# Kernel tuning notes

Measured on AMD Instinct MI355X. Metric: run time of the kernel, lower is better.

Reference implementation:

```python
import jax, jax.numpy as jnp
import numpy as np

B, S, I, H, C, V = 512, 64, 300, 1024, 2, 50000


def setup_inputs() -> dict:
    key = jax.random.key(0)
    ks = jax.random.split(key, 10)
    s = 0.05
    return {
        "x": jax.random.randint(ks[0], (B, S), 0, V),
        "lengths": jax.random.randint(ks[1], (B,), 1, S + 1),
        "embed": jax.random.normal(ks[2], (V, I), jnp.float32) * s,
        "Wih_e": jax.random.normal(ks[3], (4 * H, I), jnp.float32) * s,
        "Whh_e": jax.random.normal(ks[4], (4 * H, H), jnp.float32) * s,
        "bih_e": jnp.zeros((4 * H,), jnp.float32),
        "bhh_e": jnp.zeros((4 * H,), jnp.float32),
        "Wih_d": jax.random.normal(ks[5], (4 * H, I), jnp.float32) * s,
        "Whh_d": jax.random.normal(ks[6], (4 * H, H), jnp.float32) * s,
        "bih_d": jnp.zeros((4 * H,), jnp.float32),
        "bhh_d": jnp.zeros((4 * H,), jnp.float32),
        "W_lin": jax.random.normal(ks[7], (C, H), jnp.float32) * s,
        "b_lin": jnp.zeros((C,), jnp.float32),
    }


def lstm_cell(xi, h, c, Wih, Whh, bih, bhh):
    # PyTorch LSTMCell gate order: i, f, g, o
    g = xi @ Wih.T + bih + h @ Whh.T + bhh
    i, f, gg, o = jnp.split(g, 4, axis=-1)
    c = jax.nn.sigmoid(f) * c + jax.nn.sigmoid(i) * jnp.tanh(gg)
    return jax.nn.sigmoid(o) * jnp.tanh(c), c


def reference(x, lengths, embed, Wih_e, Whh_e, bih_e, bhh_e,
              Wih_d, Whh_d, bih_d, bhh_d, W_lin, b_lin):
    bsz, slen = x.shape
    hdim = Whh_e.shape[1]
    ncls = W_lin.shape[0]
    xs = embed[x.T]                      # [S, B, I] (seq-major, like x.transpose(0,1))

    h0 = jnp.zeros((bsz, hdim), xs.dtype)
    c0 = jnp.zeros((bsz, hdim), xs.dtype)

    def enc_step(carry, xi):
        h, c = carry
        h, c = lstm_cell(xi, h, c, Wih_e, Whh_e, bih_e, bhh_e)
        return (h, c), h

    # forward pass over sequence
    (h, c), enc_fwd = jax.lax.scan(enc_step, (h0, c0), xs)          # enc_fwd: [S,B,H]
    # backward pass with the SAME encoder cell, continuing from (h, c)
    (h, c), h_bwd = jax.lax.scan(enc_step, (h, c), xs[::-1])        # h_bwd:  [S,B,H]
    # k-th backward step pairs with encoder_forward[k] in the original code
    enc_out = (enc_fwd + h_bwd) * 0.5                               # [S,B,H]

    def dec_step(carry, xi):
        h, c = carry
        # original attention sums over batch AND hidden -> one scalar per timestep,
        # and rebuilds w as a fresh Variable (no gradient through the weights).
        w = jax.nn.softmax(jnp.sum(h[None, :, :] * enc_out, axis=(1, 2)))  # [S]
        w = jax.lax.stop_gradient(w)
        h = h + jnp.einsum('t,tbh->bh', w, enc_out)
        h, c = lstm_cell(xi, h, c, Wih_d, Whh_d, bih_d, bhh_d)
        return (h, c), h

    _, dec = jax.lax.scan(dec_step, (h, c), xs)                     # [S,B,H]

    out = dec @ W_lin.T + b_lin                                     # [S,B,C]
    out = out.transpose(1, 0, 2)                                    # [B,S,C]
    pad = jnp.array([1.0, 0.0], out.dtype)                          # overwrite beyond lengths
    mask = jnp.arange(slen)[None, :] < lengths[:, None]             # [B,S]
    out = jnp.where(mask[:, :, None], out, pad)
    return out.reshape(bsz * slen, ncls)
```

## Files before the change

### kernel.cpp

```cpp
#include <hip/hip_runtime.h>
#include <hip/hip_bf16.h>

#define BSZ 512
#define SEQ 64
#define IDIM 300
#define KP1 384
#define HDIM 1024
#define G4 4096
#define BH (BSZ*HDIM)

typedef __attribute__((ext_vector_type(8))) short bf16x8;
typedef __attribute__((ext_vector_type(4))) float f32x4;
typedef __attribute__((ext_vector_type(8))) unsigned short u16x8;
typedef __attribute__((ext_vector_type(4))) unsigned short u16x4;

__device__ __forceinline__ float sigmoidf_(float x){ return 1.f/(1.f+__expf(-x)); }
__device__ __forceinline__ float bf2f(unsigned short u){
    union{unsigned int i; float f;} v; v.i = ((unsigned)u)<<16; return v.f;
}
__device__ __forceinline__ unsigned short f2bf(float f){
    __hip_bfloat16 b = __float2bfloat16(f);
    return *(unsigned short*)&b;
}

__global__ void embed_gather_k(const int* __restrict__ x, const float* __restrict__ embed,
                               __hip_bfloat16* __restrict__ xs){
    int t = blockIdx.x, b = blockIdx.y;
    int ix = x[b*SEQ + t];
    const float* src = embed + (size_t)ix * IDIM;
    __hip_bfloat16* dst = xs + ((size_t)t*BSZ + b) * KP1;
    for (int k = threadIdx.x; k < KP1; k += 64)
        dst[k] = __float2bfloat16(k < IDIM ? src[k] : 0.f);
}

__global__ void conv_w_k(const float* __restrict__ Wih_e, const float* __restrict__ Wih_d,
                         const float* __restrict__ Whh_e, const float* __restrict__ Whh_d,
                         __hip_bfloat16* __restrict__ Pe, __hip_bfloat16* __restrict__ Pd,
                         __hip_bfloat16* __restrict__ He, __hip_bfloat16* __restrict__ Hd){
    int nr = blockIdx.x, v = blockIdx.y;
    int orig = ((nr>>5)&3)*HDIM + (nr>>7)*32 + (nr&31);
    if (v < 2){
        const float* src = (v ? Wih_d : Wih_e) + (size_t)orig*IDIM;
        __hip_bfloat16* dst = (v ? Pd : Pe) + (size_t)nr*KP1;
        for (int k = threadIdx.x; k < KP1; k += 64)
            dst[k] = __float2bfloat16(k < IDIM ? src[k] : 0.f);
    } else {
        const float* src = ((v == 3) ? Whh_d : Whh_e) + (size_t)orig*HDIM;
        __hip_bfloat16* dst = ((v == 3) ? Hd : He) + (size_t)nr*HDIM;
        for (int k = threadIdx.x; k < HDIM; k += 64)
            dst[k] = __float2bfloat16(src[k]);
    }
}

__global__ void bias_comb_k(const float* __restrict__ a, const float* __restrict__ b2,
                            const float* __restrict__ c2, const float* __restrict__ d2,
                            float* __restrict__ be, float* __restrict__ bd){
    int i = blockIdx.x*256 + threadIdx.x;
    int nr = i & 4095;
    int orig = ((nr>>5)&3)*HDIM + (nr>>7)*32 + (nr&31);
    if (i < G4) be[nr] = a[orig] + b2[orig];
    else        bd[nr] = c2[orig] + d2[orig];
}

__global__ void zero_hc_k(float* __restrict__ h, float* __restrict__ c,
                          __hip_bfloat16* __restrict__ h_bf){
    int idx = blockIdx.x*256 + threadIdx.x;
    h[idx] = 0.f; c[idx] = 0.f; h_bf[idx] = __float2bfloat16(0.f);
}

#define BM 64
#define BN 128
#define NK1 (KP1/128)
#define NK2 (HDIM/128)
#define NKT (NK1+NK2)

__global__ __launch_bounds__(512) void lstm_step_k(
    const __hip_bfloat16* __restrict__ A1, const __hip_bfloat16* __restrict__ B1,
    const __hip_bfloat16* __restrict__ A2, const __hip_bfloat16* __restrict__ B2,
    const float* __restrict__ bias,
    float* __restrict__ c, float* __restrict__ h, __hip_bfloat16* __restrict__ h_bf,
    __hip_bfloat16* __restrict__ encSlot, int mode)
{
    __shared__ __align__(16) char smem[98304];
    const int tid  = threadIdx.x;
    const int lane = tid & 63, wv = tid >> 6;
    const int row0 = blockIdx.y * BM;
    const int col0 = blockIdx.x * BN;
    const int wm = wv >> 2, wn = wv & 3;

    f32x4 acc[2][2] = {};

    auto stage = [&](int ks, int p){
        const __hip_bfloat16* A; const __hip_bfloat16* B; int KA, k0;
        if (ks < NK1){ A = A1; B = B1; KA = KP1;  k0 = ks*128; }
        else         { A = A2; B = B2; KA = HDIM; k0 = (ks-NK1)*128; }
        char* base = smem + p*49152;
        #pragma unroll
        for (int half = 0; half < 2; ++half){
            int u = half*512 + tid;
            int r = u >> 4, s = u & 15;
            int g = s ^ (r & 15);
            const __hip_bfloat16* src = A + (size_t)(row0 + r)*KA + k0 + g*8;
            char* dst = base + half*8192 + wv*1024;
            __builtin_amdgcn_global_load_lds(
                (const __attribute__((address_space(1))) void*)src,
                (__attribute__((address_space(3))) void*)dst, 16, 0, 0);
        }
        #pragma unroll
        for (int q = 0; q < 4; ++q){
            int u = q*512 + tid;
            int r = u >> 4, s = u & 15;
            int g = s ^ (r & 15);
            const __hip_bfloat16* src = B + (size_t)(col0 + r)*KA + k0 + g*8;
            char* dst = base + 16384 + q*8192 + wv*1024;
            __builtin_amdgcn_global_load_lds(
                (const __attribute__((address_space(1))) void*)src,
                (__attribute__((address_space(3))) void*)dst, 16, 0, 0);
        }
    };

    auto compute = [&](int p){
        const char* Ab = smem + p*49152;
        const char* Bb = Ab + 16384;
        const int rr = lane & 15, g = lane >> 4;
        bf16x8 af[2][4], bfr[2][4];
        #pragma unroll
        for (int m = 0; m < 2; ++m){
            int r = wm*32 + m*16 + rr;
            #pragma unroll
            for (int kk = 0; kk < 4; ++kk)
                af[m][kk] = *(const bf16x8*)(Ab + r*256 + ((kk*4 + g) ^ (r & 15))*16);
        }
        #pragma unroll
        for (int n = 0; n < 2; ++n){
            int r = wn*32 + n*16 + rr;
            #pragma unroll
            for (int kk = 0; kk < 4; ++kk)
                bfr[n][kk] = *(const bf16x8*)(Bb + r*256 + ((kk*4 + g) ^ (r & 15))*16);
        }
        #pragma unroll
        for (int kk = 0; kk < 4; ++kk)
            #pragma unroll
            for (int m = 0; m < 2; ++m)
                #pragma unroll
                for (int n = 0; n < 2; ++n)
                    acc[m][n] = __builtin_amdgcn_mfma_f32_16x16x32_bf16(af[m][kk], bfr[n][kk], acc[m][n], 0, 0, 0);
    };

    const int erow = tid >> 3;
    const int ejj0 = (tid & 7) * 4;
    const size_t ebase = (size_t)(row0 + erow)*HDIM + blockIdx.x*32 + ejj0;

    stage(0, 0);
    const f32x4 cpre = *(const f32x4*)(c + ebase);
    __syncthreads();
    for (int ks = 0; ks < NKT; ++ks){
        int p = ks & 1;
        if (ks + 1 < NKT) stage(ks + 1, p ^ 1);
        compute(p);
        __syncthreads();
    }

    float* ep = (float*)smem;
    {
        const int rr = lane & 15, q4 = lane >> 4;
        #pragma unroll
        for (int m = 0; m < 2; ++m){
            int row = wm*32 + m*16 + q4*4;
            #pragma unroll
            for (int n = 0; n < 2; ++n){
                int jj = n*16 + rr;
                float bi = bias[col0 + wn*32 + jj];
                #pragma unroll
                for (int q = 0; q < 4; ++q)
                    ep[(wn*64 + row + q)*33 + jj] = acc[m][n][q] + bi;
            }
        }
    }
    __syncthreads();
    {
        f32x4 cv, hv;
        #pragma unroll
        for (int e = 0; e < 4; ++e){
            float gi = ep[(0*64 + erow)*33 + ejj0 + e];
            float gf = ep[(1*64 + erow)*33 + ejj0 + e];
            float gg = ep[(2*64 + erow)*33 + ejj0 + e];
            float go = ep[(3*64 + erow)*33 + ejj0 + e];
            float cc = sigmoidf_(gf)*cpre[e] + sigmoidf_(gi)*tanhf(gg);
            float hh = sigmoidf_(go)*tanhf(cc);
            cv[e] = cc; hv[e] = hh;
        }
        *(f32x4*)(c + ebase) = cv;
        *(f32x4*)(h + ebase) = hv;
        u16x4 hb;
        #pragma unroll
        for (int e = 0; e < 4; ++e) hb[e] = f2bf(hv[e]);
        *(u16x4*)(h_bf + ebase) = hb;
        if (mode == 0){
            *(u16x4*)(encSlot + ebase) = hb;
        } else if (mode == 1){
            u16x4 eo = *(const u16x4*)(encSlot + ebase);
            u16x4 r;
            #pragma unroll
            for (int e = 0; e < 4; ++e) r[e] = f2bf(0.5f*(bf2f(eo[e]) + hv[e]));
            *(u16x4*)(encSlot + ebase) = r;
        }
    }
}

__global__ __launch_bounds__(256) void attn_part_k(
    const __hip_bfloat16* __restrict__ h_bf, const __hip_bfloat16* __restrict__ enc,
    float* __restrict__ part,
    const float* __restrict__ h, const float* __restrict__ Wl, const float* __restrict__ bl,
    const int* __restrict__ len, float* __restrict__ out, int dect)
{
    int lane = threadIdx.x & 63, w = threadIdx.x >> 6;
    if (blockIdx.x < 512){
        int ch = blockIdx.x & 63;
        int s0 = (blockIdx.x >> 6) * 8;
        const u16x8* hp = (const u16x8*)(h_bf + (size_t)ch*8192);
        float hf[4][8];
        #pragma unroll
        for (int k = 0; k < 4; ++k){
            u16x8 hv = hp[threadIdx.x + k*256];
            #pragma unroll
            for (int j = 0; j < 8; ++j) hf[k][j] = bf2f(hv[j]);
        }
        __shared__ float red[8][4];
        for (int si = 0; si < 8; ++si){
            const u16x8* e = (const u16x8*)(enc + (size_t)(s0 + si)*BH + (size_t)ch*8192);
            float sum = 0.f;
            #pragma unroll
            for (int k = 0; k < 4; ++k){
                u16x8 ev = e[threadIdx.x + k*256];
                #pragma unroll
                for (int j = 0; j < 8; ++j) sum += hf[k][j] * bf2f(ev[j]);
            }
            #pragma unroll
            for (int m = 32; m >= 1; m >>= 1) sum += __shfl_xor(sum, m);
            if (lane == 0) red[si][w] = sum;
        }
        __syncthreads();
        if (threadIdx.x < 8){
            int si = threadIdx.x;
            part[(s0 + si)*64 + ch] = red[si][0]+red[si][1]+red[si][2]+red[si][3];
        }
    } else if (dect >= 0){
        int b = (blockIdx.x - 512)*4 + w;
        const float* hb = h + (size_t)b*HDIM;
        float s0 = 0.f, s1 = 0.f;
        for (int j = lane; j < HDIM; j += 64){
            float v = hb[j];
            s0 += v * Wl[j];
            s1 += v * Wl[HDIM + j];
        }
        #pragma unroll
        for (int m = 32; m >= 1; m >>= 1){ s0 += __shfl_xor(s0, m); s1 += __shfl_xor(s1, m); }
        if (lane == 0){
            bool valid = dect < len[b];
            size_t r = ((size_t)b*SEQ + dect)*2;
            out[r]   = valid ? (s0 + bl[0]) : 1.0f;
            out[r+1] = valid ? (s1 + bl[1]) : 0.0f;
        }
    }
}

__global__ __launch_bounds__(256) void attn_apply_k(
    const float* __restrict__ h, const float* __restrict__ part,
    const __hip_bfloat16* __restrict__ enc, __hip_bfloat16* __restrict__ hat_bf)
{
    __shared__ float wl[64];
    int lane = threadIdx.x & 63;
    if (threadIdx.x < 64){
        float tot = 0.f;
        #pragma unroll 8
        for (int ch = 0; ch < 64; ++ch) tot += part[lane*64 + ch];
        float m = tot;
        #pragma unroll
        for (int msk = 32; msk >= 1; msk >>= 1) m = fmaxf(m, __shfl_xor(m, msk));
        float e = __expf(tot - m);
        float sm = e;
        #pragma unroll
        for (int msk = 32; msk >= 1; msk >>= 1) sm += __shfl_xor(sm, msk);
        wl[lane] = e / sm;
    }
    __syncthreads();
    size_t i4 = ((size_t)blockIdx.x*256 + threadIdx.x) * 4;
    float v[4];
    {
        f32x4 a = *(const f32x4*)(h + i4);
        v[0]=a[0]; v[1]=a[1]; v[2]=a[2]; v[3]=a[3];
    }
    for (int s = 0; s < SEQ; ++s){
        u16x4 ev = *(const u16x4*)(enc + (size_t)s*BH + i4);
        float w = wl[s];
        #pragma unroll
        for (int j = 0; j < 4; ++j) v[j] += w * bf2f(ev[j]);
    }
    u16x4 ov;
    #pragma unroll
    for (int j = 0; j < 4; ++j) ov[j] = f2bf(v[j]);
    *(u16x4*)(hat_bf + i4) = ov;
}

__global__ void dec_linear_k(const float* __restrict__ h, const float* __restrict__ Wl,
                             const float* __restrict__ bl, const int* __restrict__ len,
                             float* __restrict__ out, int t)
{
    int b = blockIdx.x, lane = threadIdx.x;
    const float* hb = h + (size_t)b*HDIM;
    float s0 = 0.f, s1 = 0.f;
    for (int j = lane; j < HDIM; j += 64){
        float v = hb[j];
        s0 += v * Wl[j];
        s1 += v * Wl[HDIM + j];
    }
    #pragma unroll
    for (int m = 32; m >= 1; m >>= 1){ s0 += __shfl_xor(s0, m); s1 += __shfl_xor(s1, m); }
    if (lane == 0){
        bool valid = t < len[b];
        size_t r = ((size_t)b*SEQ + t)*2;
        out[r]   = valid ? (s0 + bl[0]) : 1.0f;
        out[r+1] = valid ? (s1 + bl[1]) : 0.0f;
    }
}

extern "C" void kernel_launch(void* const* d_in, const int* in_sizes, int n_in,
                              void* d_out, int out_size, void* d_ws, size_t ws_size,
                              hipStream_t stream)
{
    (void)in_sizes; (void)n_in; (void)out_size; (void)ws_size;
    const int*   x      = (const int*)  d_in[0];
    const int*   len    = (const int*)  d_in[1];
    const float* embed  = (const float*)d_in[2];
    const float* Wih_e  = (const float*)d_in[3];
    const float* Whh_e  = (const float*)d_in[4];
    const float* bih_e  = (const float*)d_in[5];
    const float* bhh_e  = (const float*)d_in[6];
    const float* Wih_d  = (const float*)d_in[7];
    const float* Whh_d  = (const float*)d_in[8];
    const float* bih_d  = (const float*)d_in[9];
    const float* bhh_d  = (const float*)d_in[10];
    const float* W_lin  = (const float*)d_in[11];
    const float* b_lin  = (const float*)d_in[12];
    float* out = (float*)d_out;

    float* ws = (float*)d_ws;
    size_t off = 0;
    auto alloc = [&](size_t nfloats){ size_t o = off; off += (nfloats + 63) & ~(size_t)63; return o; };
    __hip_bfloat16* xs_bf  = (__hip_bfloat16*)(ws + alloc((size_t)SEQ*BSZ*KP1/2));
    __hip_bfloat16* Pe     = (__hip_bfloat16*)(ws + alloc((size_t)G4*KP1/2));
    __hip_bfloat16* Pd     = (__hip_bfloat16*)(ws + alloc((size_t)G4*KP1/2));
    __hip_bfloat16* He     = (__hip_bfloat16*)(ws + alloc((size_t)G4*HDIM/2));
    __hip_bfloat16* Hd     = (__hip_bfloat16*)(ws + alloc((size_t)G4*HDIM/2));
    float* be   = ws + alloc(G4);
    float* bd   = ws + alloc(G4);
    float* h    = ws + alloc(BH);
    float* c    = ws + alloc(BH);
    __hip_bfloat16* h_bf   = (__hip_bfloat16*)(ws + alloc(BH/2));
    __hip_bfloat16* hat_bf = (__hip_bfloat16*)(ws + alloc(BH/2));
    __hip_bfloat16* enc    = (__hip_bfloat16*)(ws + alloc((size_t)SEQ*BH/2));
    float* part = ws + alloc(64*64);

    embed_gather_k<<<dim3(SEQ, BSZ), 64, 0, stream>>>(x, embed, xs_bf);
    conv_w_k<<<dim3(G4, 4), 64, 0, stream>>>(Wih_e, Wih_d, Whh_e, Whh_d, Pe, Pd, He, Hd);
    bias_comb_k<<<32, 256, 0, stream>>>(bih_e, bhh_e, bih_d, bhh_d, be, bd);
    zero_hc_k<<<BH/256, 256, 0, stream>>>(h, c, h_bf);

    dim3 ggrid(G4/BN, BSZ/BM);

    for (int t = 0; t < SEQ; ++t)
        lstm_step_k<<<ggrid, 512, 0, stream>>>(xs_bf + (size_t)t*BSZ*KP1, Pe, h_bf, He, be,
                                               c, h, h_bf, enc + (size_t)t*BH, 0);
    for (int k = 0; k < SEQ; ++k){
        int t = SEQ - 1 - k;
        lstm_step_k<<<ggrid, 512, 0, stream>>>(xs_bf + (size_t)t*BSZ*KP1, Pe, h_bf, He, be,
                                               c, h, h_bf, enc + (size_t)k*BH, 1);
    }
    for (int t = 0; t < SEQ; ++t){
        attn_part_k<<<640, 256, 0, stream>>>(h_bf, enc, part, h, W_lin, b_lin, len, out, t - 1);
        attn_apply_k<<<512, 256, 0, stream>>>(h, part, enc, hat_bf);
        lstm_step_k<<<ggrid, 512, 0, stream>>>(xs_bf + (size_t)t*BSZ*KP1, Pd, hat_bf, Hd, bd,
                                               c, h, h_bf, nullptr, 2);
    }
    dec_linear_k<<<BSZ, 64, 0, stream>>>(h, W_lin, b_lin, len, out, SEQ - 1);
}
```

Before: 4.152 ms.

## Fuse attention score computation into decoder LSTM step epilogue

Computes the per-timestep attention logits (h·enc_out summed over batch and hidden) inside the decoder LSTM step epilogue, using the freshly computed h in registers. Each block writes per-block partial sums to a 64x256 buffer. The separate attn_part kernel now runs only once, before the decoder loop, and the output-linear work moves into attn_apply. This drops one kernel launch per decoder step and avoids re-reading h_bf, in exchange for a longer LSTM epilogue that streams all 64 enc slices per block and a larger partial-sum reduction.

```diff
diff --git a/kernel.cpp b/kernel.cpp
--- a/kernel.cpp
+++ b/kernel.cpp
@@ -79,7 +79,8 @@
     const __hip_bfloat16* __restrict__ A2, const __hip_bfloat16* __restrict__ B2,
     const float* __restrict__ bias,
     float* __restrict__ c, float* __restrict__ h, __hip_bfloat16* __restrict__ h_bf,
-    __hip_bfloat16* __restrict__ encSlot, int mode)
+    __hip_bfloat16* __restrict__ encSlot, int mode,
+    const __hip_bfloat16* __restrict__ enc_all, float* __restrict__ part, int logits)
 {
     __shared__ __align__(16) char smem[98304];
     const int tid  = threadIdx.x;
@@ -178,8 +179,9 @@
         }
     }
     __syncthreads();
+    f32x4 hv;
     {
-        f32x4 cv, hv;
+        f32x4 cv;
         #pragma unroll
         for (int e = 0; e < 4; ++e){
             float gi = ep[(0*64 + erow)*33 + ejj0 + e];
@@ -206,45 +208,103 @@
             *(u16x4*)(encSlot + ebase) = r;
         }
     }
+
+    if (logits){
+        __syncthreads();
+        float* lp = (float*)smem;
+        for (int s = 0; s < SEQ; ++s){
+            u16x4 ev = *(const u16x4*)(enc_all + (size_t)s*BH + ebase);
+            float p = hv[0]*bf2f(ev[0]) + hv[1]*bf2f(ev[1])
+                    + hv[2]*bf2f(ev[2]) + hv[3]*bf2f(ev[3]);
+            #pragma unroll
+            for (int m = 32; m >= 1; m >>= 1) p += __shfl_xor(p, m);
+            if (lane == 0) lp[s*8 + wv] = p;
+        }
+        __syncthreads();
+        if (tid < SEQ){
+            float t8 = 0.f;
+            #pragma unroll
+            for (int w8 = 0; w8 < 8; ++w8) t8 += lp[tid*8 + w8];
+            part[tid*256 + (blockIdx.y*32 + blockIdx.x)] = t8;
+        }
+    }
 }
 
 __global__ __launch_bounds__(256) void attn_part_k(
     const __hip_bfloat16* __restrict__ h_bf, const __hip_bfloat16* __restrict__ enc,
-    float* __restrict__ part,
-    const float* __restrict__ h, const float* __restrict__ Wl, const float* __restrict__ bl,
+    float* __restrict__ part)
+{
+    int lane = threadIdx.x & 63, w = threadIdx.x >> 6;
+    int ch = blockIdx.x & 63;
+    int s0 = (blockIdx.x >> 6) * 8;
+    const u16x8* hp = (const u16x8*)(h_bf + (size_t)ch*8192);
+    float hf[4][8];
+    #pragma unroll
+    for (int k = 0; k < 4; ++k){
+        u16x8 hv = hp[threadIdx.x + k*256];
+        #pragma unroll
+        for (int j = 0; j < 8; ++j) hf[k][j] = bf2f(hv[j]);
+    }
+    __shared__ float red[8][4];
+    for (int si = 0; si < 8; ++si){
+        const u16x8* e = (const u16x8*)(enc + (size_t)(s0 + si)*BH + (size_t)ch*8192);
+        float sum = 0.f;
+        #pragma unroll
+        for (int k = 0; k < 4; ++k){
+            u16x8 ev = e[threadIdx.x + k*256];
+            #pragma unroll
+            for (int j = 0; j < 8; ++j) sum += hf[k][j] * bf2f(ev[j]);
+        }
+        #pragma unroll
+        for (int m = 32; m >= 1; m >>= 1) sum += __shfl_xor(sum, m);
+        if (lane == 0) red[si][w] = sum;
+    }
+    __syncthreads();
+    if (threadIdx.x < 8){
+        int si = threadIdx.x;
+        part[(s0 + si)*64 + ch] = red[si][0]+red[si][1]+red[si][2]+red[si][3];
+    }
+}
+
+__global__ __launch_bounds__(256) void attn_apply_k(
+    const float* __restrict__ h, const float* __restrict__ part, int nPart,
+    const __hip_bfloat16* __restrict__ enc, __hip_bfloat16* __restrict__ hat_bf,
+    const float* __restrict__ Wl, const float* __restrict__ bl,
     const int* __restrict__ len, float* __restrict__ out, int dect)
 {
     int lane = threadIdx.x & 63, w = threadIdx.x >> 6;
     if (blockIdx.x < 512){
-        int ch = blockIdx.x & 63;
-        int s0 = (blockIdx.x >> 6) * 8;
-        const u16x8* hp = (const u16x8*)(h_bf + (size_t)ch*8192);
-        float hf[4][8];
-        #pragma unroll
-        for (int k = 0; k < 4; ++k){
-            u16x8 hv = hp[threadIdx.x + k*256];
-            #pragma unroll
-            for (int j = 0; j < 8; ++j) hf[k][j] = bf2f(hv[j]);
-        }
-        __shared__ float red[8][4];
-        for (int si = 0; si < 8; ++si){
-            const u16x8* e = (const u16x8*)(enc + (size_t)(s0 + si)*BH + (size_t)ch*8192);
-            float sum = 0.f;
-            #pragma unroll
-            for (int k = 0; k < 4; ++k){
-                u16x8 ev = e[threadIdx.x + k*256];
-                #pragma unroll
-                for (int j = 0; j < 8; ++j) sum += hf[k][j] * bf2f(ev[j]);
-            }
-            #pragma unroll
-            for (int m = 32; m >= 1; m >>= 1) sum += __shfl_xor(sum, m);
-            if (lane == 0) red[si][w] = sum;
+        __shared__ float wl[64];
+        if (threadIdx.x < 64){
+            float tot = 0.f;
+            #pragma unroll 8
+            for (int k = 0; k < nPart; ++k) tot += part[lane*nPart + k];
+            float m = tot;
+            #pragma unroll
+            for (int msk = 32; msk >= 1; msk >>= 1) m = fmaxf(m, __shfl_xor(m, msk));
+            float e = __expf(tot - m);
+            float sm = e;
+            #pragma unroll
+            for (int msk = 32; msk >= 1; msk >>= 1) sm += __shfl_xor(sm, msk);
+            wl[lane] = e / sm;
         }
         __syncthreads();
-        if (threadIdx.x < 8){
-            int si = threadIdx.x;
-            part[(s0 + si)*64 + ch] = red[si][0]+red[si][1]+red[si][2]+red[si][3];
-        }
+        size_t i4 = ((size_t)blockIdx.x*256 + threadIdx.x) * 4;
+        float v[4];
+        {
+            f32x4 a = *(const f32x4*)(h + i4);
+            v[0]=a[0]; v[1]=a[1]; v[2]=a[2]; v[3]=a[3];
+        }
+        for (int s = 0; s < SEQ; ++s){
+            u16x4 ev = *(const u16x4*)(enc + (size_t)s*BH + i4);
+            float ww = wl[s];
+            #pragma unroll
+            for (int j = 0; j < 4; ++j) v[j] += ww * bf2f(ev[j]);
+        }
+        u16x4 ov;
+        #pragma unroll
+        for (int j = 0; j < 4; ++j) ov[j] = f2bf(v[j]);
+        *(u16x4*)(hat_bf + i4) = ov;
     } else if (dect >= 0){
         int b = (blockIdx.x - 512)*4 + w;
         const float* hb = h + (size_t)b*HDIM;
@@ -263,44 +323,6 @@
             out[r+1] = valid ? (s1 + bl[1]) : 0.0f;
         }
     }
-}
-
-__global__ __launch_bounds__(256) void attn_apply_k(
-    const float* __restrict__ h, const float* __restrict__ part,
-    const __hip_bfloat16* __restrict__ enc, __hip_bfloat16* __restrict__ hat_bf)
-{
-    __shared__ float wl[64];
-    int lane = threadIdx.x & 63;
-    if (threadIdx.x < 64){
-        float tot = 0.f;
-        #pragma unroll 8
-        for (int ch = 0; ch < 64; ++ch) tot += part[lane*64 + ch];
-        float m = tot;
-        #pragma unroll
-        for (int msk = 32; msk >= 1; msk >>= 1) m = fmaxf(m, __shfl_xor(m, msk));
-        float e = __expf(tot - m);
-        float sm = e;
-        #pragma unroll
-        for (int msk = 32; msk >= 1; msk >>= 1) sm += __shfl_xor(sm, msk);
-        wl[lane] = e / sm;
-    }
-    __syncthreads();
-    size_t i4 = ((size_t)blockIdx.x*256 + threadIdx.x) * 4;
-    float v[4];
-    {
-        f32x4 a = *(const f32x4*)(h + i4);
-        v[0]=a[0]; v[1]=a[1]; v[2]=a[2]; v[3]=a[3];
-    }
-    for (int s = 0; s < SEQ; ++s){
-        u16x4 ev = *(const u16x4*)(enc + (size_t)s*BH + i4);
-        float w = wl[s];
-        #pragma unroll
-        for (int j = 0; j < 4; ++j) v[j] += w * bf2f(ev[j]);
-    }
-    u16x4 ov;
-    #pragma unroll
-    for (int j = 0; j < 4; ++j) ov[j] = f2bf(v[j]);
-    *(u16x4*)(hat_bf + i4) = ov;
 }
 
 __global__ void dec_linear_k(const float* __restrict__ h, const float* __restrict__ Wl,
@@ -360,7 +382,7 @@
     __hip_bfloat16* h_bf   = (__hip_bfloat16*)(ws + alloc(BH/2));
     __hip_bfloat16* hat_bf = (__hip_bfloat16*)(ws + alloc(BH/2));
     __hip_bfloat16* enc    = (__hip_bfloat16*)(ws + alloc((size_t)SEQ*BH/2));
-    float* part = ws + alloc(64*64);
+    float* part = ws + alloc(64*256);
 
     embed_gather_k<<<dim3(SEQ, BSZ), 64, 0, stream>>>(x, embed, xs_bf);
     conv_w_k<<<dim3(G4, 4), 64, 0, stream>>>(Wih_e, Wih_d, Whh_e, Whh_d, Pe, Pd, He, Hd);
@@ -371,17 +393,21 @@
 
     for (int t = 0; t < SEQ; ++t)
         lstm_step_k<<<ggrid, 512, 0, stream>>>(xs_bf + (size_t)t*BSZ*KP1, Pe, h_bf, He, be,
-                                               c, h, h_bf, enc + (size_t)t*BH, 0);
+                                               c, h, h_bf, enc + (size_t)t*BH, 0,
+                                               nullptr, nullptr, 0);
     for (int k = 0; k < SEQ; ++k){
         int t = SEQ - 1 - k;
         lstm_step_k<<<ggrid, 512, 0, stream>>>(xs_bf + (size_t)t*BSZ*KP1, Pe, h_bf, He, be,
-                                               c, h, h_bf, enc + (size_t)k*BH, 1);
-    }
+                                               c, h, h_bf, enc + (size_t)k*BH, 1,
+                                               nullptr, nullptr, 0);
+    }
+    attn_part_k<<<512, 256, 0, stream>>>(h_bf, enc, part);
     for (int t = 0; t < SEQ; ++t){
-        attn_part_k<<<640, 256, 0, stream>>>(h_bf, enc, part, h, W_lin, b_lin, len, out, t - 1);
-        attn_apply_k<<<512, 256, 0, stream>>>(h, part, enc, hat_bf);
+        attn_apply_k<<<640, 256, 0, stream>>>(h, part, (t == 0) ? 64 : 256, enc, hat_bf,
+                                              W_lin, b_lin, len, out, t - 1);
         lstm_step_k<<<ggrid, 512, 0, stream>>>(xs_bf + (size_t)t*BSZ*KP1, Pd, hat_bf, Hd, bd,
-                                               c, h, h_bf, nullptr, 2);
+                                               c, h, h_bf, nullptr, 2,
+                                               enc, part, (t < SEQ - 1) ? 1 : 0);
     }
     dec_linear_k<<<BSZ, 64, 0, stream>>>(h, W_lin, b_lin, len, out, SEQ - 1);
 }
```

Measured after the change: 5.921 ms. +42.6%, slower.
